# Kernel tuning notes

Hardware: AMD Instinct MI355X
Metric: run time of the kernel (lower is better)

## Reference

```python
import jax, jax.numpy as jnp
import numpy as np

B, J, T, F = 256, 8, 4096, 9


def setup_inputs() -> dict:
    key = jax.random.key(0)
    ks = jax.random.split(key, 7)
    x = jax.random.normal(ks[0], (B, J, T, F), dtype=jnp.float32)
    # Conv1d weights: [out_ch, in_ch, k], kaiming-ish scale
    w1 = jax.random.normal(ks[1], (16, 9, 3), dtype=jnp.float32) * (1.0 / np.sqrt(9 * 3))
    b1 = jax.random.normal(ks[2], (16,), dtype=jnp.float32) * 0.01
    w2 = jax.random.normal(ks[3], (32, 16, 3), dtype=jnp.float32) * (1.0 / np.sqrt(16 * 3))
    b2 = jax.random.normal(ks[4], (32,), dtype=jnp.float32) * 0.01
    w3 = jax.random.normal(ks[5], (16, 32, 3), dtype=jnp.float32) * (1.0 / np.sqrt(32 * 3))
    b3 = jax.random.normal(ks[6], (16,), dtype=jnp.float32) * 0.01
    return {"x": x, "w1": w1, "b1": b1, "w2": w2, "b2": b2, "w3": w3, "b3": b3}


def _conv_relu(h, w, b):
    # h: [N, Cin, L]; w: [Cout, Cin, 3]; padding=2 both sides (as in torch module)
    y = jax.lax.conv_general_dilated(h, w, window_strides=(1,), padding=[(2, 2)],
                                     dimension_numbers=("NCH", "OIH", "NCH"))
    return jax.nn.relu(y + b[None, :, None])


def _maxpool(h, k):
    # max pool over last dim with kernel=stride=k, floor mode (torch default)
    L = h.shape[-1] // k
    return h[..., : L * k].reshape(*h.shape[:-1], L, k).max(axis=-1)


def reference(x, w1, b1, w2, b2, w3, b3):
    b, j, t, f = x.shape
    # Fold batch*sensor-group into one conv batch dim: [B*J, 9, T]
    h = x.reshape(b * j, t, f).transpose(0, 2, 1)
    h = _maxpool(_conv_relu(h, w1, b1), 2)
    h = _maxpool(_conv_relu(h, w2, b2), 2)
    h = _maxpool(_conv_relu(h, w3, b3), 2)
    feat = h.mean(axis=2)                 # [B*J, 16]
    feat = feat.reshape(b, j * 16)        # concat over sensor groups -> [B, J*16]
    # MaxPool1d(k=3, s=3) on 2D input pools the last dim -> [B, (J*16)//3]
    return _maxpool(feat, 3)
```

## Files before the change

### kernel.cpp

```cpp
#include <hip/hip_runtime.h>

#define NS 2048
#define T 4096
#define F 9
#define CH 62
#define NCHUNK 9

#define LXP 514
#define LUP 258
#define LWP 130
#define SM_X  0
#define SM_P2 0
#define SM_P1 4640
#define SM_TOT (4640 + 16*258)

__global__ __launch_bounds__(256) __attribute__((amdgpu_waves_per_eu(4, 4)))
void fused_cnn(
    const float* __restrict__ x,
    const float* __restrict__ w1, const float* __restrict__ b1,
    const float* __restrict__ w2, const float* __restrict__ b2,
    const float* __restrict__ w3, const float* __restrict__ b3,
    float* __restrict__ feat)
{
    __shared__ float sm[SM_TOT];
    const int tid  = threadIdx.x;
    const int lane = tid & 63;
    const int wid  = tid >> 6;
    const int chunk = blockIdx.x;
    const int n     = blockIdx.y;
    const int r0 = chunk * CH;
    const int nr = min(CH, 513 - r0);
    const int nw = 2*nr + 2;
    const int nu = 4*nr + 6;
    const int nx = 8*nr + 14;

    {
        const float* xs = x + (size_t)n * (T*F);
        const int gbase = (8*r0 - 14) * F;
        const int tot = nx * F;
        for (int i = tid; i < tot; i += 256) {
            int tl = i / 9;
            int f  = i - tl*9;
            int gi = gbase + i;
            float v = (gi >= 0 && gi < T*F) ? xs[gi] : 0.f;
            sm[SM_X + f*LXP + tl] = v;
        }
    }
    __syncthreads();

    {
        const int SB = (nu + 63) >> 6;
        #pragma unroll 1
        for (int strip = 0; strip < SB; ++strip) {
            const int j = strip*64 + lane;
            const int u = 4*r0 - 6 + j;
            const bool uok = (j < nu) && (u >= 0) && (u < 2049);
            float acc0[4], acc1[4];
            #pragma unroll
            for (int ic = 0; ic < 4; ++ic) { acc0[ic] = 0.f; acc1[ic] = 0.f; }
            #pragma unroll 1
            for (int fb = 0; fb < 3; ++fb) {
                #pragma unroll
                for (int fi = 0; fi < 3; ++fi) {
                    const int f_ = fb*3 + fi;
                    const float* xw = sm + SM_X + f_*LXP + 2*j;
                    float x0 = xw[0], x1 = xw[1], x2 = xw[2], x3 = xw[3];
                    #pragma unroll
                    for (int ic = 0; ic < 4; ++ic) {
                        const int cu = __builtin_amdgcn_readfirstlane(wid + 4*ic);
                        const float* wp = w1 + cu*27 + fb*9 + fi*3;
                        float wv0 = wp[0], wv1 = wp[1], wv2 = wp[2];
                        acc0[ic] = fmaf(x0, wv0, acc0[ic]);
                        acc1[ic] = fmaf(x1, wv0, acc1[ic]);
                        acc0[ic] = fmaf(x1, wv1, acc0[ic]);
                        acc1[ic] = fmaf(x2, wv1, acc1[ic]);
                        acc0[ic] = fmaf(x2, wv2, acc0[ic]);
                        acc1[ic] = fmaf(x3, wv2, acc1[ic]);
                    }
                }
            }
            #pragma unroll
            for (int ic = 0; ic < 4; ++ic) {
                const int cu = __builtin_amdgcn_readfirstlane(wid + 4*ic);
                const float bc = b1[cu];
                float res = uok ? fmaxf(fmaxf(acc0[ic] + bc, acc1[ic] + bc), 0.f) : 0.f;
                if (j < nu) sm[SM_P1 + cu*LUP + j] = res;
            }
        }
    }
    __syncthreads();

    {
        const int SC = (nw + 63) >> 6;
        #pragma unroll 1
        for (int strip = 0; strip < SC; ++strip) {
            const int m = strip*64 + lane;
            const int w = 2*r0 - 2 + m;
            const bool wok = (m < nw) && (w >= 0) && (w < 1025);
            float acc0[8], acc1[8];
            #pragma unroll
            for (int io = 0; io < 8; ++io) { acc0[io] = 0.f; acc1[io] = 0.f; }
            #pragma unroll 1
            for (int cb = 0; cb < 8; ++cb) {
                #pragma unroll
                for (int cq = 0; cq < 2; ++cq) {
                    const int ci = cb*2 + cq;
                    const float* pw = sm + SM_P1 + ci*LUP + 2*m;
                    float p0 = pw[0], p1 = pw[1], p2v = pw[2], p3 = pw[3];
                    #pragma unroll
                    for (int io = 0; io < 8; ++io) {
                        const int ou = __builtin_amdgcn_readfirstlane(wid + 4*io);
                        const float* wp = w2 + ou*48 + ci*3;
                        float wv0 = wp[0], wv1 = wp[1], wv2 = wp[2];
                        acc0[io] = fmaf(p0,  wv0, acc0[io]);
                        acc1[io] = fmaf(p1,  wv0, acc1[io]);
                        acc0[io] = fmaf(p1,  wv1, acc0[io]);
                        acc1[io] = fmaf(p2v, wv1, acc1[io]);
                        acc0[io] = fmaf(p2v, wv2, acc0[io]);
                        acc1[io] = fmaf(p3,  wv2, acc1[io]);
                    }
                }
            }
            #pragma unroll
            for (int io = 0; io < 8; ++io) {
                const int ou = __builtin_amdgcn_readfirstlane(wid + 4*io);
                const float bo = b2[ou];
                float res = wok ? fmaxf(fmaxf(acc0[io] + bo, acc1[io] + bo), 0.f) : 0.f;
                if (m < nw) sm[SM_P2 + ou*LWP + m] = res;
            }
        }
    }
    __syncthreads();

    {
        const bool rok = (lane < nr);
        float acc0[4], acc1[4];
        #pragma unroll
        for (int io = 0; io < 4; ++io) { acc0[io] = 0.f; acc1[io] = 0.f; }
        #pragma unroll 1
        for (int cb = 0; cb < 8; ++cb) {
            #pragma unroll
            for (int cq = 0; cq < 4; ++cq) {
                const int ci = cb*4 + cq;
                const float* pw = sm + SM_P2 + ci*LWP + 2*lane;
                float p0 = pw[0], p1 = pw[1], p2v = pw[2], p3 = pw[3];
                #pragma unroll
                for (int io = 0; io < 4; ++io) {
                    const int ou = __builtin_amdgcn_readfirstlane(wid + 4*io);
                    const float* wp = w3 + ou*96 + ci*3;
                    float wv0 = wp[0], wv1 = wp[1], wv2 = wp[2];
                    acc0[io] = fmaf(p0,  wv0, acc0[io]);
                    acc1[io] = fmaf(p1,  wv0, acc1[io]);
                    acc0[io] = fmaf(p1,  wv1, acc0[io]);
                    acc1[io] = fmaf(p2v, wv1, acc1[io]);
                    acc0[io] = fmaf(p2v, wv2, acc0[io]);
                    acc1[io] = fmaf(p3,  wv2, acc1[io]);
                }
            }
        }
        #pragma unroll
        for (int io = 0; io < 4; ++io) {
            const int ou = __builtin_amdgcn_readfirstlane(wid + 4*io);
            const float bo = b3[ou];
            float v = fmaxf(fmaxf(acc0[io] + bo, acc1[io] + bo), 0.f);
            v = rok ? v : 0.f;
            #pragma unroll
            for (int off = 32; off >= 1; off >>= 1)
                v += __shfl_down(v, off, 64);
            if (lane == 0) atomicAdd(&feat[n*16 + ou], v);
        }
    }
}

__global__ void finalize_kernel(const float* __restrict__ feat, float* __restrict__ out) {
    int i = blockIdx.x * blockDim.x + threadIdx.x;
    if (i < 256*42) {
        int b = i / 42;
        int q = i - b*42;
        const float* f = feat + b*128 + q*3;
        out[i] = fmaxf(fmaxf(f[0], f[1]), f[2]) * (1.0f/513.0f);
    }
}

extern "C" void kernel_launch(void* const* d_in, const int* in_sizes, int n_in,
                              void* d_out, int out_size, void* d_ws, size_t ws_size,
                              hipStream_t stream) {
    const float* x  = (const float*)d_in[0];
    const float* w1 = (const float*)d_in[1];
    const float* b1 = (const float*)d_in[2];
    const float* w2 = (const float*)d_in[3];
    const float* b2 = (const float*)d_in[4];
    const float* w3 = (const float*)d_in[5];
    const float* b3 = (const float*)d_in[6];
    float* feat = (float*)d_ws;
    hipMemsetAsync(feat, 0, NS*16*sizeof(float), stream);
    dim3 grid(NCHUNK, NS);
    fused_cnn<<<grid, 256, 0, stream>>>(x, w1, b1, w2, b2, w3, b3, feat);
    finalize_kernel<<<(256*42 + 255)/256, 256, 0, stream>>>(feat, (float*)d_out);
}
```

Before: 882.4 us.

## Use packed v2f FMAs and hoist weights across strips in conv stages

```diff
diff --git a/kernel.cpp b/kernel.cpp
--- a/kernel.cpp
+++ b/kernel.cpp
@@ -5,6 +5,8 @@
 #define F 9
 #define CH 62
 #define NCHUNK 9
+
+typedef float v2f __attribute__((ext_vector_type(2)));
 
 #define LXP 514
 #define LUP 258
@@ -49,112 +51,149 @@
     __syncthreads();
 
     {
-        const int SB = (nu + 63) >> 6;
+        v2f acc[4][4];
+        #pragma unroll
+        for (int s = 0; s < 4; ++s)
+            #pragma unroll
+            for (int ic = 0; ic < 4; ++ic) acc[s][ic] = (v2f){0.f, 0.f};
         #pragma unroll 1
-        for (int strip = 0; strip < SB; ++strip) {
-            const int j = strip*64 + lane;
-            const int u = 4*r0 - 6 + j;
-            const bool uok = (j < nu) && (u >= 0) && (u < 2049);
-            float acc0[4], acc1[4];
-            #pragma unroll
-            for (int ic = 0; ic < 4; ++ic) { acc0[ic] = 0.f; acc1[ic] = 0.f; }
-            #pragma unroll 1
-            for (int fb = 0; fb < 3; ++fb) {
-                #pragma unroll
-                for (int fi = 0; fi < 3; ++fi) {
-                    const int f_ = fb*3 + fi;
-                    const float* xw = sm + SM_X + f_*LXP + 2*j;
-                    float x0 = xw[0], x1 = xw[1], x2 = xw[2], x3 = xw[3];
+        for (int fb = 0; fb < 3; ++fb) {
+            float wv[3][4][3];
+            #pragma unroll
+            for (int fi = 0; fi < 3; ++fi)
+                #pragma unroll
+                for (int ic = 0; ic < 4; ++ic) {
+                    const int cu = __builtin_amdgcn_readfirstlane(wid + 4*ic);
+                    const float* wp = w1 + cu*27 + (fb*3 + fi)*3;
+                    wv[fi][ic][0] = wp[0]; wv[fi][ic][1] = wp[1]; wv[fi][ic][2] = wp[2];
+                }
+            #pragma unroll
+            for (int s = 0; s < 4; ++s) {
+                if (s*64 < nu) {
+                    const int j = s*64 + lane;
                     #pragma unroll
-                    for (int ic = 0; ic < 4; ++ic) {
-                        const int cu = __builtin_amdgcn_readfirstlane(wid + 4*ic);
-                        const float* wp = w1 + cu*27 + fb*9 + fi*3;
-                        float wv0 = wp[0], wv1 = wp[1], wv2 = wp[2];
-                        acc0[ic] = fmaf(x0, wv0, acc0[ic]);
-                        acc1[ic] = fmaf(x1, wv0, acc1[ic]);
-                        acc0[ic] = fmaf(x1, wv1, acc0[ic]);
-                        acc1[ic] = fmaf(x2, wv1, acc1[ic]);
-                        acc0[ic] = fmaf(x2, wv2, acc0[ic]);
-                        acc1[ic] = fmaf(x3, wv2, acc1[ic]);
+                    for (int fi = 0; fi < 3; ++fi) {
+                        const float* xw = sm + SM_X + (fb*3 + fi)*LXP + 2*j;
+                        float x0 = xw[0], x1 = xw[1], x2 = xw[2], x3 = xw[3];
+                        v2f p01 = {x0, x1}, p12 = {x1, x2}, p23 = {x2, x3};
+                        #pragma unroll
+                        for (int ic = 0; ic < 4; ++ic) {
+                            v2f w0s = {wv[fi][ic][0], wv[fi][ic][0]};
+                            v2f w1s = {wv[fi][ic][1], wv[fi][ic][1]};
+                            v2f w2s = {wv[fi][ic][2], wv[fi][ic][2]};
+                            acc[s][ic] = __builtin_elementwise_fma(p01, w0s, acc[s][ic]);
+                            acc[s][ic] = __builtin_elementwise_fma(p12, w1s, acc[s][ic]);
+                            acc[s][ic] = __builtin_elementwise_fma(p23, w2s, acc[s][ic]);
+                        }
                     }
                 }
             }
-            #pragma unroll
-            for (int ic = 0; ic < 4; ++ic) {
-                const int cu = __builtin_amdgcn_readfirstlane(wid + 4*ic);
-                const float bc = b1[cu];
-                float res = uok ? fmaxf(fmaxf(acc0[ic] + bc, acc1[ic] + bc), 0.f) : 0.f;
-                if (j < nu) sm[SM_P1 + cu*LUP + j] = res;
+        }
+        #pragma unroll
+        for (int s = 0; s < 4; ++s) {
+            if (s*64 < nu) {
+                const int j = s*64 + lane;
+                const int u = 4*r0 - 6 + j;
+                const bool uok = (j < nu) && (u >= 0) && (u < 2049);
+                #pragma unroll
+                for (int ic = 0; ic < 4; ++ic) {
+                    const int cu = __builtin_amdgcn_readfirstlane(wid + 4*ic);
+                    const float bc = b1[cu];
+                    float res = uok ? fmaxf(fmaxf(acc[s][ic].x + bc, acc[s][ic].y + bc), 0.f) : 0.f;
+                    if (j < nu) sm[SM_P1 + cu*LUP + j] = res;
+                }
             }
         }
     }
     __syncthreads();
 
     {
-        const int SC = (nw + 63) >> 6;
-        #pragma unroll 1
-        for (int strip = 0; strip < SC; ++strip) {
-            const int m = strip*64 + lane;
-            const int w = 2*r0 - 2 + m;
-            const bool wok = (m < nw) && (w >= 0) && (w < 1025);
-            float acc0[8], acc1[8];
-            #pragma unroll
-            for (int io = 0; io < 8; ++io) { acc0[io] = 0.f; acc1[io] = 0.f; }
-            #pragma unroll 1
-            for (int cb = 0; cb < 8; ++cb) {
-                #pragma unroll
-                for (int cq = 0; cq < 2; ++cq) {
-                    const int ci = cb*2 + cq;
-                    const float* pw = sm + SM_P1 + ci*LUP + 2*m;
-                    float p0 = pw[0], p1 = pw[1], p2v = pw[2], p3 = pw[3];
-                    #pragma unroll
-                    for (int io = 0; io < 8; ++io) {
-                        const int ou = __builtin_amdgcn_readfirstlane(wid + 4*io);
-                        const float* wp = w2 + ou*48 + ci*3;
-                        float wv0 = wp[0], wv1 = wp[1], wv2 = wp[2];
-                        acc0[io] = fmaf(p0,  wv0, acc0[io]);
-                        acc1[io] = fmaf(p1,  wv0, acc1[io]);
-                        acc0[io] = fmaf(p1,  wv1, acc0[io]);
-                        acc1[io] = fmaf(p2v, wv1, acc1[io]);
-                        acc0[io] = fmaf(p2v, wv2, acc0[io]);
-                        acc1[io] = fmaf(p3,  wv2, acc1[io]);
-                    }
-                }
-            }
-            #pragma unroll
-            for (int io = 0; io < 8; ++io) {
-                const int ou = __builtin_amdgcn_readfirstlane(wid + 4*io);
-                const float bo = b2[ou];
-                float res = wok ? fmaxf(fmaxf(acc0[io] + bo, acc1[io] + bo), 0.f) : 0.f;
-                if (m < nw) sm[SM_P2 + ou*LWP + m] = res;
-            }
-        }
-    }
-    __syncthreads();
-
-    {
-        const bool rok = (lane < nr);
-        float acc0[4], acc1[4];
-        #pragma unroll
-        for (int io = 0; io < 4; ++io) { acc0[io] = 0.f; acc1[io] = 0.f; }
+        v2f acc[2][8];
+        #pragma unroll
+        for (int s = 0; s < 2; ++s)
+            #pragma unroll
+            for (int io = 0; io < 8; ++io) acc[s][io] = (v2f){0.f, 0.f};
         #pragma unroll 1
         for (int cb = 0; cb < 8; ++cb) {
-            #pragma unroll
-            for (int cq = 0; cq < 4; ++cq) {
-                const int ci = cb*4 + cq;
-                const float* pw = sm + SM_P2 + ci*LWP + 2*lane;
-                float p0 = pw[0], p1 = pw[1], p2v = pw[2], p3 = pw[3];
+            float wv[2][8][3];
+            #pragma unroll
+            for (int cq = 0; cq < 2; ++cq)
+                #pragma unroll
+                for (int io = 0; io < 8; ++io) {
+                    const int ou = __builtin_amdgcn_readfirstlane(wid + 4*io);
+                    const float* wp = w2 + ou*48 + (cb*2 + cq)*3;
+                    wv[cq][io][0] = wp[0]; wv[cq][io][1] = wp[1]; wv[cq][io][2] = wp[2];
+                }
+            #pragma unroll
+            for (int s = 0; s < 2; ++s) {
+                if (s*64 < nw) {
+                    const int m = s*64 + lane;
+                    #pragma unroll
+                    for (int cq = 0; cq < 2; ++cq) {
+                        const float* pw = sm + SM_P1 + (cb*2 + cq)*LUP + 2*m;
+                        float p0 = pw[0], p1 = pw[1], p2v = pw[2], p3 = pw[3];
+                        v2f q01 = {p0, p1}, q12 = {p1, p2v}, q23 = {p2v, p3};
+                        #pragma unroll
+                        for (int io = 0; io < 8; ++io) {
+                            v2f w0s = {wv[cq][io][0], wv[cq][io][0]};
+                            v2f w1s = {wv[cq][io][1], wv[cq][io][1]};
+                            v2f w2s = {wv[cq][io][2], wv[cq][io][2]};
+                            acc[s][io] = __builtin_elementwise_fma(q01, w0s, acc[s][io]);
+                            acc[s][io] = __builtin_elementwise_fma(q12, w1s, acc[s][io]);
+                            acc[s][io] = __builtin_elementwise_fma(q23, w2s, acc[s][io]);
+                        }
+                    }
+                }
+            }
+        }
+        __syncthreads();
+        #pragma unroll
+        for (int s = 0; s < 2; ++s) {
+            if (s*64 < nw) {
+                const int m = s*64 + lane;
+                const int w = 2*r0 - 2 + m;
+                const bool wok = (m < nw) && (w >= 0) && (w < 1025);
+                #pragma unroll
+                for (int io = 0; io < 8; ++io) {
+                    const int ou = __builtin_amdgcn_readfirstlane(wid + 4*io);
+                    const float bo = b2[ou];
+                    float res = wok ? fmaxf(fmaxf(acc[s][io].x + bo, acc[s][io].y + bo), 0.f) : 0.f;
+                    if (m < nw) sm[SM_P2 + ou*LWP + m] = res;
+                }
+            }
+        }
+    }
+    __syncthreads();
+
+    {
+        const bool rok = (lane < nr);
+        v2f acc[4];
+        #pragma unroll
+        for (int io = 0; io < 4; ++io) acc[io] = (v2f){0.f, 0.f};
+        #pragma unroll 1
+        for (int cb = 0; cb < 8; ++cb) {
+            float wv[4][4][3];
+            #pragma unroll
+            for (int cq = 0; cq < 4; ++cq)
                 #pragma unroll
                 for (int io = 0; io < 4; ++io) {
                     const int ou = __builtin_amdgcn_readfirstlane(wid + 4*io);
-                    const float* wp = w3 + ou*96 + ci*3;
-                    float wv0 = wp[0], wv1 = wp[1], wv2 = wp[2];
-                    acc0[io] = fmaf(p0,  wv0, acc0[io]);
-                    acc1[io] = fmaf(p1,  wv0, acc1[io]);
-                    acc0[io] = fmaf(p1,  wv1, acc0[io]);
-                    acc1[io] = fmaf(p2v, wv1, acc1[io]);
-                    acc0[io] = fmaf(p2v, wv2, acc0[io]);
-                    acc1[io] = fmaf(p3,  wv2, acc1[io]);
+                    const float* wp = w3 + ou*96 + (cb*4 + cq)*3;
+                    wv[cq][io][0] = wp[0]; wv[cq][io][1] = wp[1]; wv[cq][io][2] = wp[2];
+                }
+            #pragma unroll
+            for (int cq = 0; cq < 4; ++cq) {
+                const float* pw = sm + SM_P2 + (cb*4 + cq)*LWP + 2*lane;
+                float p0 = pw[0], p1 = pw[1], p2v = pw[2], p3 = pw[3];
+                v2f q01 = {p0, p1}, q12 = {p1, p2v}, q23 = {p2v, p3};
+                #pragma unroll
+                for (int io = 0; io < 4; ++io) {
+                    v2f w0s = {wv[cq][io][0], wv[cq][io][0]};
+                    v2f w1s = {wv[cq][io][1], wv[cq][io][1]};
+                    v2f w2s = {wv[cq][io][2], wv[cq][io][2]};
+                    acc[io] = __builtin_elementwise_fma(q01, w0s, acc[io]);
+                    acc[io] = __builtin_elementwise_fma(q12, w1s, acc[io]);
+                    acc[io] = __builtin_elementwise_fma(q23, w2s, acc[io]);
                 }
             }
         }
@@ -162,7 +201,7 @@
         for (int io = 0; io < 4; ++io) {
             const int ou = __builtin_amdgcn_readfirstlane(wid + 4*io);
             const float bo = b3[ou];
-            float v = fmaxf(fmaxf(acc0[io] + bo, acc1[io] + bo), 0.f);
+            float v = fmaxf(fmaxf(acc[io].x + bo, acc[io].y + bo), 0.f);
             v = rok ? v : 0.f;
             #pragma unroll
             for (int off = 32; off >= 1; off >>= 1)
```

Result: faster. 782.5 us (-11.3%).
